# Kernel optimization log

Hardware: AMD Instinct MI355X
Metric: run time of the kernel (lower is better)

Reference implementation:

```python
import jax, jax.numpy as jnp
import numpy as np

B, N, F_IN, F_OUT, T, E, K = 8, 1024, 32, 64, 24, 16384, 3


def setup_inputs() -> dict:
    key = jax.random.key(0)
    ks = jax.random.split(key, 9)
    return {
        "x": jax.random.normal(ks[0], (B, N, F_IN, T), jnp.float32),
        "edge_index": jax.random.randint(ks[1], (2, E), 0, N),
        "edge_weight": jax.random.uniform(ks[2], (E,), jnp.float32),
        # attention params (xavier-ish scale)
        "Ve": jax.random.normal(ks[3], (T, T), jnp.float32) * 0.2,
        "be": jax.random.normal(ks[4], (1, T, T), jnp.float32) * 0.2,
        "Vs": jax.random.normal(ks[5], (N, N), jnp.float32) * 0.03,
        "bs": jax.random.normal(ks[6], (1, N, N), jnp.float32) * 0.03,
        # ChebConv: K linear layers (no bias) + shared bias
        "cheb_W": jax.random.normal(ks[7], (K, F_IN, F_OUT), jnp.float32) * (1.0 / np.sqrt(F_IN)),
        "cheb_b": jnp.zeros((F_OUT,), jnp.float32),
        # 1x1 residual Conv2d(F_IN -> F_OUT): weight (F_OUT, F_IN), bias (F_OUT,)
        "res_W": jax.random.normal(ks[8], (F_OUT, F_IN), jnp.float32) * (1.0 / np.sqrt(F_IN)),
        "res_b": jnp.zeros((F_OUT,), jnp.float32),
    }


def _cheb_conv(x, row, col, w, Wk, b):
    """PyG-style ChebConv applied to a batch of graphs sharing edges.
    x: (BT, N, Fin). Scaled Laplacian with lambda_max=2 reduces to
    L_hat = -D^{-1/2} A D^{-1/2} with zero diagonal (self-loops removed).
    """
    n = x.shape[1]
    w = jnp.where(row == col, jnp.zeros_like(w), w)  # remove_self_loops
    deg = jnp.zeros((n,), x.dtype).at[row].add(w)
    dis = jnp.where(deg > 0, jax.lax.rsqrt(jnp.where(deg > 0, deg, 1.0)), 0.0)
    norm = -dis[row] * w * dis[col]  # (E,)

    def prop(z):  # z: (BT, N, F) -> L_hat @ z
        msg = norm[None, :, None] * z[:, row, :]  # (BT, E, F)
        return jnp.zeros_like(z).at[:, col, :].add(msg)

    Tx0 = x
    out = Tx0 @ Wk[0]
    Tx1 = prop(Tx0)
    out = out + Tx1 @ Wk[1]
    for k in range(2, Wk.shape[0]):  # small fixed K, not a data-dim loop
        Tx2 = 2.0 * prop(Tx1) - Tx0
        out = out + Tx2 @ Wk[k]
        Tx0, Tx1 = Tx1, Tx2
    return out + b


def reference(x, edge_index, edge_weight, Ve, be, Vs, bs, cheb_W, cheb_b, res_W, res_b):
    b_, n, f, t = x.shape
    row, col = edge_index[0], edge_index[1]

    # --- temporal attention: E = softmax(Ve @ sigmoid(X^T X) + be) ---
    x_flat = x.reshape(b_, n * f, t)
    score_t = jnp.einsum('bmt,bmu->btu', x_flat, x_flat)
    E_att = jax.nn.softmax(jnp.einsum('tu,buv->btv', Ve, jax.nn.sigmoid(score_t)) + be, axis=-1)
    x_TA = (x_flat @ E_att).reshape(b_, n, f, t)

    # --- spatial attention: S = softmax(Vs @ sigmoid(X X^T) + bs) ---
    xr = x_TA.reshape(b_, n, f * t)
    score_s = jnp.einsum('bnd,bmd->bnm', xr, xr)
    S_att = jax.nn.softmax(jnp.einsum('nm,bmk->bnk', Vs, jax.nn.sigmoid(score_s)) + bs, axis=-1)
    x_SA = (S_att @ xr).reshape(b_, n, f, t)

    # --- Chebyshev graph conv, batched over all B*T slices at once ---
    xg = x_SA.transpose(0, 3, 1, 2).reshape(b_ * t, n, f)  # (BT, N, Fin)
    x_gcn = _cheb_conv(xg, row, col, edge_weight, cheb_W, cheb_b)
    x_gcn = x_gcn.reshape(b_, t, n, -1).transpose(0, 2, 3, 1)  # (B, N, Fout, T)

    # --- 1x1 residual conv over channel dim ---
    x_res = jnp.einsum('gf,bnft->bngt', res_W, x) + res_b[None, None, :, None]

    return jax.nn.relu(x_gcn + x_res)
```

## Files before the change

kernel.cpp:

```cpp
#include <hip/hip_runtime.h>
#include <math.h>

#define NB 1024
#define FB 32
#define TB 24
#define GB 64
#define BB 8
#define EB 16384
#define MB 32768
#define DB 768
#define BTB 192
#define WSP 6144

typedef __attribute__((ext_vector_type(8))) short sh8;
typedef __attribute__((ext_vector_type(4))) float f32x4;

__device__ __forceinline__ float wsum(float v){
  #pragma unroll
  for (int o = 32; o; o >>= 1) v += __shfl_down(v, o);
  return v;
}
__device__ __forceinline__ float wmax(float v){
  #pragma unroll
  for (int o = 32; o; o >>= 1) v = fmaxf(v, __shfl_down(v, o));
  return v;
}
__device__ __forceinline__ float sigm(float v){ return 1.f / (1.f + expf(-v)); }
__device__ __forceinline__ float b2f(unsigned short u){ unsigned int t = ((unsigned int)u) << 16; return __uint_as_float(t); }
__device__ __forceinline__ unsigned short f2b(float f){
  unsigned int u = __float_as_uint(f);
  u += 0x7fffu + ((u >> 16) & 1u);
  return (unsigned short)(u >> 16);
}
__device__ __forceinline__ void gload16(const void* g, void* l){
  typedef const __attribute__((address_space(1))) unsigned int* gp_t;
  typedef __attribute__((address_space(3))) unsigned int* lp_t;
  __builtin_amdgcn_global_load_lds((gp_t)g, (lp_t)l, 16, 0, 0);
}

__global__ __launch_bounds__(256) void k_pass1(const float* __restrict__ x,
                                               unsigned short* __restrict__ xTn,
                                               float* __restrict__ score){
  const int n0 = blockIdx.x * 8, b = blockIdx.y;
  __shared__ float xl[8 * 32 * 25];
  const float* src = x + ((size_t)b * NB + n0) * DB;
  #pragma unroll
  for (int p = 0; p < 24; ++p){
    int i = p * 256 + threadIdx.x;
    int n = i / 768, rem = i % 768, f = rem / 24, t = rem % 24;
    xl[(n * 32 + f) * 25 + t] = src[i];
  }
  __syncthreads();
  #pragma unroll
  for (int nn = 0; nn < 8; ++nn){
    unsigned short* dst = xTn + ((size_t)(n0 + nn) * BTB + b * TB) * FB;
    #pragma unroll
    for (int p = 0; p < 3; ++p){
      int i2 = p * 256 + threadIdx.x;
      int t = i2 >> 5, f = i2 & 31;
      dst[t * FB + f] = f2b(xl[(nn * 32 + f) * 25 + t]);
    }
  }
  if (threadIdx.x < 192){
    const int t = threadIdx.x >> 3, u0 = (threadIdx.x & 7) * 3;
    float a0 = 0.f, a1 = 0.f, a2 = 0.f;
    for (int m = 0; m < 256; ++m){
      const float xt = xl[m * 25 + t];
      a0 = fmaf(xt, xl[m * 25 + u0 + 0], a0);
      a1 = fmaf(xt, xl[m * 25 + u0 + 1], a1);
      a2 = fmaf(xt, xl[m * 25 + u0 + 2], a2);
    }
    float* sb = score + (size_t)b * 576 + t * 24 + u0;
    atomicAdd(sb + 0, a0); atomicAdd(sb + 1, a1); atomicAdd(sb + 2, a2);
  }
}

__global__ __launch_bounds__(64) void k_eatt(const float* __restrict__ score,
                                             const float* __restrict__ Ve,
                                             const float* __restrict__ be,
                                             float* __restrict__ Eatt){
  const int b = blockIdx.x;
  __shared__ float sg[576], Ar[576], Vel[576], bel[576];
  for (int i = threadIdx.x; i < 576; i += 64){
    sg[i] = sigm(score[(size_t)b * 576 + i]);
    Vel[i] = Ve[i]; bel[i] = be[i];
  }
  __syncthreads();
  for (int i = threadIdx.x; i < 576; i += 64){
    int t = i / 24, v = i % 24;
    float s = 0.f;
    #pragma unroll
    for (int u = 0; u < 24; ++u) s = fmaf(Vel[t*24+u], sg[u*24+v], s);
    Ar[i] = s + bel[i];
  }
  __syncthreads();
  if (threadIdx.x < 24){
    const int t = threadIdx.x;
    float mx = -1e30f;
    #pragma unroll
    for (int v = 0; v < 24; ++v) mx = fmaxf(mx, Ar[t*24+v]);
    float e[24]; float sum = 0.f;
    #pragma unroll
    for (int v = 0; v < 24; ++v){ e[v] = expf(Ar[t*24+v] - mx); sum += e[v]; }
    const float inv = 1.f / sum;
    #pragma unroll
    for (int v = 0; v < 24; ++v) Eatt[(size_t)b * 576 + t*24 + v] = e[v] * inv;
  }
}

__global__ __launch_bounds__(256) void k_xta2(const unsigned short* __restrict__ xTn,
                                              const float* __restrict__ Eatt,
                                              unsigned short* __restrict__ xTAh){
  const int n0 = blockIdx.x * 8, b = blockIdx.y;
  __shared__ float E[576];
  __shared__ unsigned short xl[8 * 32 * 25];
  for (int i = threadIdx.x; i < 576; i += 256) E[i] = Eatt[(size_t)b * 576 + i];
  #pragma unroll
  for (int p = 0; p < 12; ++p){
    int i = p * 256 + threadIdx.x;
    int nn = i / 384, within = i % 384;
    unsigned int v = *(const unsigned int*)(xTn + ((size_t)(n0 + nn) * BTB + b * TB) * FB + within * 2);
    int e0 = within * 2, t0 = e0 >> 5, f0 = e0 & 31;
    int e1 = e0 + 1,     t1 = e1 >> 5, f1 = e1 & 31;
    xl[(nn * 32 + f0) * 25 + t0] = (unsigned short)v;
    xl[(nn * 32 + f1) * 25 + t1] = (unsigned short)(v >> 16);
  }
  __syncthreads();
  const int r = threadIdx.x;
  float in[TB], o[TB];
  #pragma unroll
  for (int u = 0; u < TB; ++u) in[u] = b2f(xl[r * 25 + u]);
  #pragma unroll
  for (int v = 0; v < TB; ++v) o[v] = 0.f;
  #pragma unroll
  for (int u = 0; u < TB; ++u){
    const float xv = in[u];
    #pragma unroll
    for (int v = 0; v < TB; ++v) o[v] = fmaf(xv, E[u*24+v], o[v]);
  }
  unsigned int pk[12];
  #pragma unroll
  for (int q = 0; q < 12; ++q)
    pk[q] = (unsigned int)f2b(o[2*q]) | ((unsigned int)f2b(o[2*q+1]) << 16);
  uint4* op = (uint4*)(xTAh + ((size_t)b * MB + n0 * 32 + r) * TB);
  op[0] = make_uint4(pk[0], pk[1], pk[2], pk[3]);
  op[1] = make_uint4(pk[4], pk[5], pk[6], pk[7]);
  op[2] = make_uint4(pk[8], pk[9], pk[10], pk[11]);
}

__global__ __launch_bounds__(256) void k_tr(const unsigned short* __restrict__ in,
                                            unsigned short* __restrict__ out){
  const int dt = blockIdx.x, nt = blockIdx.y, b = blockIdx.z;
  __shared__ unsigned short ts[64 * 66];
  const unsigned short* ib = in + (size_t)b * (NB * DB) + (size_t)(nt * 64) * DB + dt * 64;
  #pragma unroll
  for (int p = 0; p < 8; ++p){
    int fl = p * 256 + threadIdx.x;
    int rr = fl >> 5, cc = (fl & 31) * 2;
    unsigned int v = *(const unsigned int*)(ib + (size_t)rr * DB + cc);
    ts[rr * 66 + cc] = (unsigned short)v;
    ts[rr * 66 + cc + 1] = (unsigned short)(v >> 16);
  }
  __syncthreads();
  unsigned short* ob = out + (size_t)b * (NB * DB) + (size_t)(dt * 64) * NB + nt * 64;
  #pragma unroll
  for (int p = 0; p < 16; ++p){
    int fl = p * 256 + threadIdx.x;
    int dd = fl >> 6, nn = fl & 63;
    ob[(size_t)dd * NB + nn] = ts[nn * 66 + dd];
  }
}

template<int EPI>
__global__ __launch_bounds__(256, 3) void k_mgemm(const unsigned short* __restrict__ A,
                                                  const unsigned short* __restrict__ B,
                                                  unsigned short* __restrict__ C,
                                                  int lda, int ldb, int ldc, int Kk, int nbx,
                                                  long sA, long sB, long sC){
  __shared__ unsigned short As[8192];
  __shared__ unsigned short Bs[8192];
  const int d = blockIdx.x;
  const int bz = d & 7;
  const int rr = d >> 3;
  const int bx = rr % nbx, by = rr / nbx;
  A += (size_t)bz * sA; B += (size_t)bz * sB; C += (size_t)bz * sC;
  const int i0 = by * 128, j0 = bx * 128;
  const int tid = threadIdx.x, wave = tid >> 6, lane = tid & 63;
  const int fr = lane & 15, rowb = (lane >> 4) * 4;
  const int wr = (wave >> 1) * 64, wc = (wave & 1) * 64;
  const int srow = tid >> 3;
  const int sko = (((lane & 7) ^ (lane >> 3)) * 8);
  f32x4 acc[4][4];
  #pragma unroll
  for (int m = 0; m < 4; ++m)
    #pragma unroll
    for (int n = 0; n < 4; ++n) acc[m][n] = 0.f;

  for (int k0 = 0; k0 < Kk; k0 += 64){
    #pragma unroll
    for (int it = 0; it < 4; ++it){
      const int r = it * 32 + srow;
      gload16(A + (size_t)(i0 + r) * lda + k0 + sko, &As[(it*4 + wave) * 512]);
      gload16(B + (size_t)(j0 + r) * ldb + k0 + sko, &Bs[(it*4 + wave) * 512]);
    }
    asm volatile("s_waitcnt vmcnt(0)" ::: "memory");
    __syncthreads();
    #pragma unroll
    for (int kk = 0; kk < 2; ++kk){
      const int ch = kk * 4 + (lane >> 4);
      const int cs = (ch ^ (fr & 7)) * 8;
      sh8 af[4], bfr[4];
      #pragma unroll
      for (int m = 0; m < 4; ++m)
        af[m] = *(const sh8*)&As[(wr + m*16 + fr) * 64 + cs];
      #pragma unroll
      for (int n = 0; n < 4; ++n)
        bfr[n] = *(const sh8*)&Bs[(wc + n*16 + fr) * 64 + cs];
      #pragma unroll
      for (int m = 0; m < 4; ++m)
        #pragma unroll
        for (int n = 0; n < 4; ++n)
          acc[m][n] = __builtin_amdgcn_mfma_f32_16x16x32_bf16(af[m], bfr[n], acc[m][n], 0, 0, 0);
    }
    __syncthreads();
  }

  #pragma unroll
  for (int m = 0; m < 4; ++m){
    const int row = i0 + wr + m*16 + rowb;
    #pragma unroll
    for (int n = 0; n < 4; ++n){
      const int colg = j0 + wc + n*16 + fr;
      #pragma unroll
      for (int r = 0; r < 4; ++r){
        float v = acc[m][n][r];
        if (EPI == 1) v = sigm(v);
        C[(size_t)(row + r) * ldc + colg] = f2b(v);
      }
    }
  }
}

__global__ __launch_bounds__(256) void k_softmax_s(const unsigned short* __restrict__ C2h,
                                                   const float* __restrict__ bs,
                                                   unsigned short* __restrict__ Sh){
  const int blk = blockIdx.x;
  const int n = blk & 1023;
  const unsigned short* row = C2h + (size_t)blk * 1024;
  const float* bsr = bs + (size_t)n * 1024;
  const int tid = threadIdx.x;
  uint2 rv = ((const uint2*)row)[tid];
  float4 bb = ((const float4*)bsr)[tid];
  float v0 = b2f((unsigned short)rv.x)         + bb.x;
  float v1 = b2f((unsigned short)(rv.x >> 16)) + bb.y;
  float v2 = b2f((unsigned short)rv.y)         + bb.z;
  float v3 = b2f((unsigned short)(rv.y >> 16)) + bb.w;
  float mx = fmaxf(fmaxf(v0, v1), fmaxf(v2, v3));
  mx = wmax(mx);
  __shared__ float s4[4];
  __shared__ float s4b[4];
  if ((tid & 63) == 0) s4[tid >> 6] = mx;
  __syncthreads();
  mx = fmaxf(fmaxf(s4[0], s4[1]), fmaxf(s4[2], s4[3]));
  float e0 = expf(v0 - mx), e1 = expf(v1 - mx), e2 = expf(v2 - mx), e3 = expf(v3 - mx);
  float sum = wsum(e0 + e1 + e2 + e3);
  if ((tid & 63) == 0) s4b[tid >> 6] = sum;
  __syncthreads();
  sum = s4b[0] + s4b[1] + s4b[2] + s4b[3];
  const float inv = 1.f / sum;
  uint2 ov;
  ov.x = (unsigned int)f2b(e0 * inv) | ((unsigned int)f2b(e1 * inv) << 16);
  ov.y = (unsigned int)f2b(e2 * inv) | ((unsigned int)f2b(e3 * inv) << 16);
  ((uint2*)(Sh + (size_t)blk * 1024))[tid] = ov;
}

__global__ __launch_bounds__(256) void k_t0n(const unsigned short* __restrict__ xSAh,
                                             unsigned short* __restrict__ T0n){
  const int n0 = blockIdx.x * 8, b = blockIdx.y;
  __shared__ unsigned short s[8 * 32 * 25];
  const unsigned int* src = (const unsigned int*)(xSAh + ((size_t)b * NB + n0) * DB);
  #pragma unroll
  for (int p = 0; p < 12; ++p){
    int i = p * 256 + threadIdx.x;
    unsigned int v = src[i];
    int d0 = (i * 2) % DB, nn = (i * 2) / DB;
    int f0 = d0 / 24, t0 = d0 % 24;
    int d1 = d0 + 1, f1 = d1 / 24, t1 = d1 % 24;
    s[(nn * 32 + f0) * 25 + t0] = (unsigned short)v;
    s[(nn * 32 + f1) * 25 + t1] = (unsigned short)(v >> 16);
  }
  __syncthreads();
  #pragma unroll
  for (int nn = 0; nn < 8; ++nn){
    unsigned short* dst = T0n + ((size_t)(n0 + nn) * BTB + b * TB) * FB;
    #pragma unroll
    for (int p = 0; p < 3; ++p){
      int i2 = p * 256 + threadIdx.x;
      int t = i2 >> 5, f = i2 & 31;
      dst[t * FB + f] = s[(nn * 32 + f) * 25 + t];
    }
  }
}

__global__ __launch_bounds__(256) void k_edge_deg(const int* __restrict__ ei,
                                                  const float* __restrict__ ew,
                                                  float* __restrict__ deg,
                                                  int* __restrict__ cnt){
  int e = blockIdx.x * 256 + threadIdx.x;
  if (e >= EB) return;
  int r = ei[e], c = ei[EB + e];
  float w = (r == c) ? 0.f : ew[e];
  atomicAdd(&deg[r], w);
  atomicAdd(&cnt[c], 1);
}

__global__ __launch_bounds__(1024) void k_scan(const int* __restrict__ cnt,
                                               int* __restrict__ ptr,
                                               int* __restrict__ fill){
  __shared__ int sd[1024];
  const int i = threadIdx.x;
  int c = cnt[i];
  sd[i] = c;
  __syncthreads();
  int v = c;
  for (int s = 1; s < 1024; s <<= 1){
    int t = (i >= s) ? sd[i - s] : 0;
    __syncthreads();
    v += t; sd[i] = v;
    __syncthreads();
  }
  ptr[i + 1] = v;
  fill[i] = v - c;
  if (i == 0) ptr[0] = 0;
}

__global__ __launch_bounds__(256) void k_edge_fill(const int* __restrict__ ei,
                                                   const float* __restrict__ ew,
                                                   const float* __restrict__ deg,
                                                   int* __restrict__ fill,
                                                   int* __restrict__ cidx,
                                                   float* __restrict__ normv){
  int e = blockIdx.x * 256 + threadIdx.x;
  if (e >= EB) return;
  int r = ei[e], c = ei[EB + e];
  float w = (r == c) ? 0.f : ew[e];
  float dr = deg[r], dc = deg[c];
  float ir = dr > 0.f ? rsqrtf(dr) : 0.f;
  float ic = dc > 0.f ? rsqrtf(dc) : 0.f;
  normv[e] = -ir * w * ic;
  int pos = atomicAdd(&fill[c], 1);
  cidx[pos] = e;
}

#define ACC8W(vv, wv) { \
  acc[0] = fmaf(wv, b2f((unsigned short)(vv).x), acc[0]); \
  acc[1] = fmaf(wv, b2f((unsigned short)((vv).x >> 16)), acc[1]); \
  acc[2] = fmaf(wv, b2f((unsigned short)(vv).y), acc[2]); \
  acc[3] = fmaf(wv, b2f((unsigned short)((vv).y >> 16)), acc[3]); \
  acc[4] = fmaf(wv, b2f((unsigned short)(vv).z), acc[4]); \
  acc[5] = fmaf(wv, b2f((unsigned short)((vv).z >> 16)), acc[5]); \
  acc[6] = fmaf(wv, b2f((unsigned short)(vv).w), acc[6]); \
  acc[7] = fmaf(wv, b2f((unsigned short)((vv).w >> 16)), acc[7]); }

__global__ __launch_bounds__(192) void k_spmm(const unsigned short* __restrict__ z,
                                              const float* __restrict__ normv,
                                              const int* __restrict__ cidx,
                                              const int* __restrict__ ei,
                                              const int* __restrict__ ptr,
                                              const unsigned short* __restrict__ sub,
                                              float scale,
                                              unsigned short* __restrict__ outz){
  const int s = blockIdx.x & 3;
  const int c = blockIdx.x >> 2;
  const int off = s * 1536 + threadIdx.x * 8;
  const int j0 = ptr[c], j1 = ptr[c + 1];
  __shared__ int rs[192];
  __shared__ float ws[192];
  float acc[8] = {0.f, 0.f, 0.f, 0.f, 0.f, 0.f, 0.f, 0.f};
  for (int jb = j0; jb < j1; jb += 192){
    const int cnt = min(192, j1 - jb);
    __syncthreads();
    if (threadIdx.x < cnt){
      int e = cidx[jb + threadIdx.x];
      rs[threadIdx.x] = ei[e];
      ws[threadIdx.x] = normv[e];
    }
    __syncthreads();
    int j = 0;
    for (; j + 8 <= cnt; j += 8){
      uint4 v0 = *(const uint4*)(z + (size_t)rs[j+0] * WSP + off);
      uint4 v1 = *(const uint4*)(z + (size_t)rs[j+1] * WSP + off);
      uint4 v2 = *(const uint4*)(z + (size_t)rs[j+2] * WSP + off);
      uint4 v3 = *(const uint4*)(z + (size_t)rs[j+3] * WSP + off);
      uint4 v4 = *(const uint4*)(z + (size_t)rs[j+4] * WSP + off);
      uint4 v5 = *(const uint4*)(z + (size_t)rs[j+5] * WSP + off);
      uint4 v6 = *(const uint4*)(z + (size_t)rs[j+6] * WSP + off);
      uint4 v7 = *(const uint4*)(z + (size_t)rs[j+7] * WSP + off);
      float w0 = ws[j+0], w1 = ws[j+1], w2 = ws[j+2], w3 = ws[j+3];
      float w4 = ws[j+4], w5 = ws[j+5], w6 = ws[j+6], w7 = ws[j+7];
      ACC8W(v0, w0) ACC8W(v1, w1) ACC8W(v2, w2) ACC8W(v3, w3)
      ACC8W(v4, w4) ACC8W(v5, w5) ACC8W(v6, w6) ACC8W(v7, w7)
    }
    if (j + 4 <= cnt){
      uint4 v0 = *(const uint4*)(z + (size_t)rs[j+0] * WSP + off);
      uint4 v1 = *(const uint4*)(z + (size_t)rs[j+1] * WSP + off);
      uint4 v2 = *(const uint4*)(z + (size_t)rs[j+2] * WSP + off);
      uint4 v3 = *(const uint4*)(z + (size_t)rs[j+3] * WSP + off);
      float w0 = ws[j+0], w1 = ws[j+1], w2 = ws[j+2], w3 = ws[j+3];
      ACC8W(v0, w0) ACC8W(v1, w1) ACC8W(v2, w2) ACC8W(v3, w3)
      j += 4;
    }
    for (; j < cnt; ++j){
      const uint4 v = *(const uint4*)(z + (size_t)rs[j] * WSP + off);
      const float w = ws[j];
      ACC8W(v, w)
    }
  }
  float sv[8] = {0.f, 0.f, 0.f, 0.f, 0.f, 0.f, 0.f, 0.f};
  if (sub){
    const uint4 s0 = *(const uint4*)(sub + (size_t)c * WSP + off);
    sv[0]=b2f((unsigned short)s0.x); sv[1]=b2f((unsigned short)(s0.x>>16));
    sv[2]=b2f((unsigned short)s0.y); sv[3]=b2f((unsigned short)(s0.y>>16));
    sv[4]=b2f((unsigned short)s0.z); sv[5]=b2f((unsigned short)(s0.z>>16));
    sv[6]=b2f((unsigned short)s0.w); sv[7]=b2f((unsigned short)(s0.w>>16));
  }
  unsigned int pk[4];
  #pragma unroll
  for (int q = 0; q < 4; ++q){
    float a = scale * acc[2*q]     - sv[2*q];
    float b = scale * acc[2*q + 1] - sv[2*q + 1];
    pk[q] = (unsigned int)f2b(a) | ((unsigned int)f2b(b) << 16);
  }
  *(uint4*)(outz + (size_t)c * WSP + off) = make_uint4(pk[0], pk[1], pk[2], pk[3]);
}

__global__ __launch_bounds__(256) void k_fgemm(const unsigned short* __restrict__ T0n,
                                               const unsigned short* __restrict__ T1n,
                                               const unsigned short* __restrict__ T2n,
                                               const unsigned short* __restrict__ xTn,
                                               const unsigned short* __restrict__ Wh,
                                               const float* __restrict__ bsum,
                                               float* __restrict__ out){
  __shared__ unsigned short As[16384];
  __shared__ unsigned short Ws[8192];
  const int m0 = blockIdx.x * 128;
  const int tid = threadIdx.x, wave = tid >> 6, lane = tid & 63;
  const int fr = lane & 15, rowb = (lane >> 4) * 4;
  const int wr = (wave >> 1) * 64, wc = (wave & 1) * 32;
  #pragma unroll
  for (int it = 0; it < 8; ++it){
    const int row = it * 16 + wave * 4 + (lane >> 4);
    const int g = (lane & 15) ^ (row & 7);
    const int ss = g >> 2, off = (g & 3) * 8;
    const unsigned short* bp = (ss == 0) ? T0n : (ss == 1) ? T1n : (ss == 2) ? T2n : xTn;
    gload16(bp + (size_t)(m0 + row) * FB + off, &As[(it*4 + wave) * 512]);
  }
  #pragma unroll
  for (int it = 0; it < 4; ++it){
    const int row = it * 16 + wave * 4 + (lane >> 4);
    const int g = (lane & 15) ^ (row & 7);
    gload16(Wh + (size_t)row * 128 + g * 8, &Ws[(it*4 + wave) * 512]);
  }
  __syncthreads();
  f32x4 acc[4][2];
  #pragma unroll
  for (int m = 0; m < 4; ++m){ acc[m][0] = 0.f; acc[m][1] = 0.f; }
  #pragma unroll
  for (int kk = 0; kk < 4; ++kk){
    const int ch = kk * 4 + (lane >> 4);
    const int cs = (ch ^ (fr & 7)) * 8;
    sh8 af[4], bf2[2];
    #pragma unroll
    for (int m = 0; m < 4; ++m)
      af[m] = *(const sh8*)&As[(wr + m*16 + fr) * 128 + cs];
    #pragma unroll
    for (int n = 0; n < 2; ++n)
      bf2[n] = *(const sh8*)&Ws[(wc + n*16 + fr) * 128 + cs];
    #pragma unroll
    for (int m = 0; m < 4; ++m)
      #pragma unroll
      for (int n = 0; n < 2; ++n)
        acc[m][n] = __builtin_amdgcn_mfma_f32_16x16x32_bf16(af[m], bf2[n], acc[m][n], 0, 0, 0);
  }
  #pragma unroll
  for (int m = 0; m < 4; ++m){
    const int row4 = m0 + wr + m*16 + rowb;
    const int nn = row4 / 192;
    const int rem = row4 - nn * 192;
    const int b = rem / 24;
    const int t0 = rem - b * 24;
    #pragma unroll
    for (int n = 0; n < 2; ++n){
      const int g = wc + n*16 + fr;
      const float bv = bsum[g];
      float4 v;
      v.x = fmaxf(acc[m][n][0] + bv, 0.f);
      v.y = fmaxf(acc[m][n][1] + bv, 0.f);
      v.z = fmaxf(acc[m][n][2] + bv, 0.f);
      v.w = fmaxf(acc[m][n][3] + bv, 0.f);
      *(float4*)(out + (((size_t)b * NB + nn) * GB + g) * TB + t0) = v;
    }
  }
}

__global__ __launch_bounds__(256) void k_const(const float* __restrict__ Vs,
                                               const float* __restrict__ cW,
                                               const float* __restrict__ cB,
                                               const float* __restrict__ rW,
                                               const float* __restrict__ rB,
                                               unsigned short* __restrict__ Vsh,
                                               unsigned short* __restrict__ Wh,
                                               float* __restrict__ bsum){
  if (blockIdx.x == 0){
    for (int i = threadIdx.x; i < 8192; i += 256){
      int g = i >> 7, k = i & 127;
      int s = k >> 5, f = k & 31;
      float v = (s < 3) ? cW[(s * 32 + f) * 64 + g] : rW[g * 32 + f];
      Wh[i] = f2b(v);
    }
    if (threadIdx.x < 64) bsum[threadIdx.x] = cB[threadIdx.x] + rB[threadIdx.x];
  } else {
    int i = ((blockIdx.x - 1) * 256 + threadIdx.x) * 4;
    float4 v = *(const float4*)(Vs + i);
    unsigned short* o = Vsh + i;
    o[0] = f2b(v.x); o[1] = f2b(v.y); o[2] = f2b(v.z); o[3] = f2b(v.w);
  }
}

extern "C" void kernel_launch(void* const* d_in, const int* in_sizes, int n_in,
                              void* d_out, int out_size, void* d_ws, size_t ws_size,
                              hipStream_t stream){
  const float* x  = (const float*)d_in[0];
  const int*   ei = (const int*)d_in[1];
  const float* ew = (const float*)d_in[2];
  const float* Ve = (const float*)d_in[3];
  const float* be = (const float*)d_in[4];
  const float* Vs = (const float*)d_in[5];
  const float* bs = (const float*)d_in[6];
  const float* cW = (const float*)d_in[7];
  const float* cB = (const float*)d_in[8];
  const float* rW = (const float*)d_in[9];
  const float* rB = (const float*)d_in[10];
  float* out = (float*)d_out;

  char* W = (char*)d_ws;
  unsigned short* sigh  = (unsigned short*)(W + 0);
  unsigned short* Sh    = sigh;
  unsigned short* xTAh  = (unsigned short*)(W + 16777216);
  unsigned short* T0n   = xTAh;
  unsigned short* xTAhT = (unsigned short*)(W + 29360128);
  unsigned short* T1n   = xTAhT;
  unsigned short* xTn   = (unsigned short*)(W + 41943040);
  unsigned short* xSAh  = (unsigned short*)(W + 54525952);
  unsigned short* T2n   = xSAh;
  unsigned short* C2h   = (unsigned short*)(W + 67108864);
  unsigned short* Vsh   = (unsigned short*)(W + 83886080);
  unsigned short* Wh    = (unsigned short*)(W + 92274688);
  float* bsum  = (float*)(W + 92291072);
  float* score = (float*)(W + 92291328);
  float* Eatt  = (float*)(W + 92309760);
  float* normv = (float*)(W + 92328192);
  float* deg   = (float*)(W + 92393728);
  int*   cnt   = (int*)(W + 92397824);
  int*   ptr   = (int*)(W + 92401920);
  int*   fill  = (int*)(W + 92406272);
  int*   cidx  = (int*)(W + 92410368);

  hipMemsetAsync(score, 0, 18432, stream);
  hipMemsetAsync(deg, 0, 8192, stream);

  k_const<<<1025, 256, 0, stream>>>(Vs, cW, cB, rW, rB, Vsh, Wh, bsum);

  k_pass1<<<dim3(128, 8), 256, 0, stream>>>(x, xTn, score);
  k_eatt<<<8, 64, 0, stream>>>(score, Ve, be, Eatt);
  k_xta2<<<dim3(128, 8), 256, 0, stream>>>(xTn, Eatt, xTAh);
  k_tr<<<dim3(12, 16, 8), 256, 0, stream>>>(xTAh, xTAhT);

  k_mgemm<1><<<512, 256, 0, stream>>>(xTAh, xTAh, sigh, DB, DB, NB, DB, 8,
                                      (long)NB*DB, (long)NB*DB, (long)NB*NB);
  k_mgemm<2><<<512, 256, 0, stream>>>(Vsh, sigh, C2h, NB, NB, NB, NB, 8,
                                      0L, (long)NB*NB, (long)NB*NB);
  k_softmax_s<<<8192, 256, 0, stream>>>(C2h, bs, Sh);
  k_mgemm<2><<<384, 256, 0, stream>>>(Sh, xTAhT, xSAh, NB, NB, DB, NB, 6,
                                      (long)NB*NB, (long)NB*DB, (long)NB*DB);

  k_t0n<<<dim3(128, 8), 256, 0, stream>>>(xSAh, T0n);
  k_edge_deg<<<64, 256, 0, stream>>>(ei, ew, deg, cnt);
  k_scan<<<1, 1024, 0, stream>>>(cnt, ptr, fill);
  k_edge_fill<<<64, 256, 0, stream>>>(ei, ew, deg, fill, cidx, normv);
  k_spmm<<<4096, 192, 0, stream>>>(T0n, normv, cidx, ei, ptr, nullptr, 1.f, T1n);
  k_spmm<<<4096, 192, 0, stream>>>(T1n, normv, cidx, ei, ptr, T0n, 2.f, T2n);

  k_fgemm<<<1536, 256, 0, stream>>>(T0n, T1n, T2n, xTn, Wh, bsum, out);
}
```

Measured before the change: 221.4 us.

## Fuse temporal-attention softmax into xta2 and graph preprocessing into one block

The E-attention computation moves into k_xta2, so every block recomputes the 24x24 sigmoid, matmul and softmax from score instead of a separate k_eatt launch writing Eatt. The three graph-preprocessing kernels (degree, scan, fill) become a single 1024-thread block that does its atomics in shared memory. The two memsets are replaced by zeroing score inside k_const. The aim is fewer launches and less global atomic traffic, at the cost of redundant attention work in each xta2 block and a serial single-block graph kernel.

New measurement: 230.2 us. 1.04x slower.

```diff
diff --git a/kernel.cpp b/kernel.cpp
--- a/kernel.cpp
+++ b/kernel.cpp
@@ -75,23 +75,22 @@
   }
 }
 
-__global__ __launch_bounds__(64) void k_eatt(const float* __restrict__ score,
-                                             const float* __restrict__ Ve,
-                                             const float* __restrict__ be,
-                                             float* __restrict__ Eatt){
-  const int b = blockIdx.x;
-  __shared__ float sg[576], Ar[576], Vel[576], bel[576];
-  for (int i = threadIdx.x; i < 576; i += 64){
-    sg[i] = sigm(score[(size_t)b * 576 + i]);
-    Vel[i] = Ve[i]; bel[i] = be[i];
-  }
-  __syncthreads();
-  for (int i = threadIdx.x; i < 576; i += 64){
+__global__ __launch_bounds__(256) void k_xta2(const unsigned short* __restrict__ xTn,
+                                              const float* __restrict__ score,
+                                              const float* __restrict__ Ve,
+                                              const float* __restrict__ be,
+                                              unsigned short* __restrict__ xTAh){
+  const int n0 = blockIdx.x * 8, b = blockIdx.y;
+  __shared__ float E[576], sg[576], Ar[576];
+  __shared__ unsigned short xl[8 * 32 * 25];
+  for (int i = threadIdx.x; i < 576; i += 256) sg[i] = sigm(score[(size_t)b * 576 + i]);
+  __syncthreads();
+  for (int i = threadIdx.x; i < 576; i += 256){
     int t = i / 24, v = i % 24;
     float s = 0.f;
     #pragma unroll
-    for (int u = 0; u < 24; ++u) s = fmaf(Vel[t*24+u], sg[u*24+v], s);
-    Ar[i] = s + bel[i];
+    for (int u = 0; u < 24; ++u) s = fmaf(Ve[t*24+u], sg[u*24+v], s);
+    Ar[i] = s + be[i];
   }
   __syncthreads();
   if (threadIdx.x < 24){
@@ -104,17 +103,8 @@
     for (int v = 0; v < 24; ++v){ e[v] = expf(Ar[t*24+v] - mx); sum += e[v]; }
     const float inv = 1.f / sum;
     #pragma unroll
-    for (int v = 0; v < 24; ++v) Eatt[(size_t)b * 576 + t*24 + v] = e[v] * inv;
-  }
-}
-
-__global__ __launch_bounds__(256) void k_xta2(const unsigned short* __restrict__ xTn,
-                                              const float* __restrict__ Eatt,
-                                              unsigned short* __restrict__ xTAh){
-  const int n0 = blockIdx.x * 8, b = blockIdx.y;
-  __shared__ float E[576];
-  __shared__ unsigned short xl[8 * 32 * 25];
-  for (int i = threadIdx.x; i < 576; i += 256) E[i] = Eatt[(size_t)b * 576 + i];
+    for (int v = 0; v < 24; ++v) E[t*24 + v] = e[v] * inv;
+  }
   #pragma unroll
   for (int p = 0; p < 12; ++p){
     int i = p * 256 + threadIdx.x;
@@ -302,24 +292,28 @@
   }
 }
 
-__global__ __launch_bounds__(256) void k_edge_deg(const int* __restrict__ ei,
-                                                  const float* __restrict__ ew,
-                                                  float* __restrict__ deg,
-                                                  int* __restrict__ cnt){
-  int e = blockIdx.x * 256 + threadIdx.x;
-  if (e >= EB) return;
-  int r = ei[e], c = ei[EB + e];
-  float w = (r == c) ? 0.f : ew[e];
-  atomicAdd(&deg[r], w);
-  atomicAdd(&cnt[c], 1);
-}
-
-__global__ __launch_bounds__(1024) void k_scan(const int* __restrict__ cnt,
-                                               int* __restrict__ ptr,
-                                               int* __restrict__ fill){
+__global__ __launch_bounds__(1024) void k_graph(const int* __restrict__ ei,
+                                                const float* __restrict__ ew,
+                                                int* __restrict__ ptr,
+                                                int* __restrict__ cidx,
+                                                float* __restrict__ normv){
+  __shared__ float degs[1024];
+  __shared__ int cnts[1024];
+  __shared__ int base[1024];
   __shared__ int sd[1024];
   const int i = threadIdx.x;
-  int c = cnt[i];
+  degs[i] = 0.f; cnts[i] = 0;
+  __syncthreads();
+  #pragma unroll
+  for (int p = 0; p < 16; ++p){
+    int e = p * 1024 + i;
+    int r = ei[e], c = ei[EB + e];
+    float w = (r == c) ? 0.f : ew[e];
+    atomicAdd(&degs[r], w);
+    atomicAdd(&cnts[c], 1);
+  }
+  __syncthreads();
+  int c = cnts[i];
   sd[i] = c;
   __syncthreads();
   int v = c;
@@ -330,26 +324,21 @@
     __syncthreads();
   }
   ptr[i + 1] = v;
-  fill[i] = v - c;
+  base[i] = v - c;
   if (i == 0) ptr[0] = 0;
-}
-
-__global__ __launch_bounds__(256) void k_edge_fill(const int* __restrict__ ei,
-                                                   const float* __restrict__ ew,
-                                                   const float* __restrict__ deg,
-                                                   int* __restrict__ fill,
-                                                   int* __restrict__ cidx,
-                                                   float* __restrict__ normv){
-  int e = blockIdx.x * 256 + threadIdx.x;
-  if (e >= EB) return;
-  int r = ei[e], c = ei[EB + e];
-  float w = (r == c) ? 0.f : ew[e];
-  float dr = deg[r], dc = deg[c];
-  float ir = dr > 0.f ? rsqrtf(dr) : 0.f;
-  float ic = dc > 0.f ? rsqrtf(dc) : 0.f;
-  normv[e] = -ir * w * ic;
-  int pos = atomicAdd(&fill[c], 1);
-  cidx[pos] = e;
+  __syncthreads();
+  #pragma unroll
+  for (int p = 0; p < 16; ++p){
+    int e = p * 1024 + i;
+    int r = ei[e], cc = ei[EB + e];
+    float w = (r == cc) ? 0.f : ew[e];
+    float dr = degs[r], dc = degs[cc];
+    float ir = dr > 0.f ? rsqrtf(dr) : 0.f;
+    float ic = dc > 0.f ? rsqrtf(dc) : 0.f;
+    normv[e] = -ir * w * ic;
+    int pos = atomicAdd(&base[cc], 1);
+    cidx[pos] = e;
+  }
 }
 
 #define ACC8W(vv, wv) { \
@@ -510,7 +499,8 @@
                                                const float* __restrict__ rB,
                                                unsigned short* __restrict__ Vsh,
                                                unsigned short* __restrict__ Wh,
-                                               float* __restrict__ bsum){
+                                               float* __restrict__ bsum,
+                                               float* __restrict__ score){
   if (blockIdx.x == 0){
     for (int i = threadIdx.x; i < 8192; i += 256){
       int g = i >> 7, k = i & 127;
@@ -519,6 +509,7 @@
       Wh[i] = f2b(v);
     }
     if (threadIdx.x < 64) bsum[threadIdx.x] = cB[threadIdx.x] + rB[threadIdx.x];
+    for (int i = threadIdx.x; i < 4608; i += 256) score[i] = 0.f;
   } else {
     int i = ((blockIdx.x - 1) * 256 + threadIdx.x) * 4;
     float4 v = *(const float4*)(Vs + i);
@@ -558,22 +549,15 @@
   unsigned short* Wh    = (unsigned short*)(W + 92274688);
   float* bsum  = (float*)(W + 92291072);
   float* score = (float*)(W + 92291328);
-  float* Eatt  = (float*)(W + 92309760);
   float* normv = (float*)(W + 92328192);
-  float* deg   = (float*)(W + 92393728);
-  int*   cnt   = (int*)(W + 92397824);
   int*   ptr   = (int*)(W + 92401920);
-  int*   fill  = (int*)(W + 92406272);
   int*   cidx  = (int*)(W + 92410368);
 
-  hipMemsetAsync(score, 0, 18432, stream);
-  hipMemsetAsync(deg, 0, 8192, stream);
-
-  k_const<<<1025, 256, 0, stream>>>(Vs, cW, cB, rW, rB, Vsh, Wh, bsum);
+  k_const<<<1025, 256, 0, stream>>>(Vs, cW, cB, rW, rB, Vsh, Wh, bsum, score);
+  k_graph<<<1, 1024, 0, stream>>>(ei, ew, ptr, cidx, normv);
 
   k_pass1<<<dim3(128, 8), 256, 0, stream>>>(x, xTn, score);
-  k_eatt<<<8, 64, 0, stream>>>(score, Ve, be, Eatt);
-  k_xta2<<<dim3(128, 8), 256, 0, stream>>>(xTn, Eatt, xTAh);
+  k_xta2<<<dim3(128, 8), 256, 0, stream>>>(xTn, score, Ve, be, xTAh);
   k_tr<<<dim3(12, 16, 8), 256, 0, stream>>>(xTAh, xTAhT);
 
   k_mgemm<1><<<512, 256, 0, stream>>>(xTAh, xTAh, sigh, DB, DB, NB, DB, 8,
@@ -585,9 +569,6 @@
                                       (long)NB*NB, (long)NB*DB, (long)NB*DB);
 
   k_t0n<<<dim3(128, 8), 256, 0, stream>>>(xSAh, T0n);
-  k_edge_deg<<<64, 256, 0, stream>>>(ei, ew, deg, cnt);
-  k_scan<<<1, 1024, 0, stream>>>(cnt, ptr, fill);
-  k_edge_fill<<<64, 256, 0, stream>>>(ei, ew, deg, fill, cidx, normv);
   k_spmm<<<4096, 192, 0, stream>>>(T0n, normv, cidx, ei, ptr, nullptr, 1.f, T1n);
   k_spmm<<<4096, 192, 0, stream>>>(T1n, normv, cidx, ei, ptr, T0n, 2.f, T2n);
 
```
